# Kernel optimization log

Measured on AMD Instinct MI355X. Metric: run time of the kernel, lower is better.

Reference implementation:

```python
import jax, jax.numpy as jnp
import numpy as np

K_NN = 32          # configs['k']
LEAKY_ALPHA = 0.2  # configs['alpha']
NHEADS = 8         # all heads share gat_W0/gat_a0 in the weights dict -> tiled output
NEG_INF = -9e15    # masked-softmax fill used by dense GAT


@jax.custom_vjp
def grad_reverse(x):
    # GradientReversalLayer: identity forward, negated gradient backward
    return x

def _gr_fwd(x):
    return x, None

def _gr_bwd(res, g):
    return (-g,)

grad_reverse.defvjp(_gr_fwd, _gr_bwd)


def setup_inputs() -> dict:
    key = jax.random.key(0)
    ks = jax.random.split(key, 11)
    N, D = 6144, 512           # N = (num_domains+1)*batch_size = 4*1536
    H1, H2, G = 256, 128, 64   # hidden_layers=[256,128], gat_hidden=[64]
    C, ND = 16, 3              # num_classes, num source-domain discriminators

    def xav(k, shape):
        limit = np.float32(np.sqrt(6.0 / (shape[0] + shape[1])) * 1.414)
        return jax.random.uniform(k, shape, jnp.float32, -limit, limit)

    return {
        "x": jax.random.normal(ks[0], (N, D), jnp.float32),
        "fc_W0": xav(ks[1], (D, H1)),
        "fc_b0": jax.random.normal(ks[2], (H1,), jnp.float32) * 0.01,
        "fc_W1": xav(ks[3], (H1, H2)),
        "fc_b1": jax.random.normal(ks[4], (H2,), jnp.float32) * 0.01,
        "gat_W": xav(ks[5], (H2, G)),
        "gat_a": jax.random.normal(ks[6], (2 * G, 1), jnp.float32) * 0.1,
        "cls_W": xav(ks[7], (NHEADS * G, C)),
        "cls_b": jax.random.normal(ks[8], (C,), jnp.float32) * 0.01,
        "dsc_W": jax.random.uniform(ks[9], (ND, NHEADS * G, 2), jnp.float32),
        "dsc_b": jax.random.uniform(ks[10], (ND, 2), jnp.float32),
    }


def reference(x, fc_W0, fc_b0, fc_W1, fc_b1, gat_W, gat_a, cls_W, cls_b, dsc_W, dsc_b):
    # --- feature extractor MLP (Linear 'fc' + relu), dropout=0 / eval mode ---
    h = jax.nn.relu(x @ fc_W0 + fc_b0)
    h = jax.nn.relu(h @ fc_W1 + fc_b1)          # [N, 128]
    n = h.shape[0]

    # --- AdjacencyLayer / DistanceLayer: kNN over pairwise L2 distances ---
    sq = jnp.sum(h * h, axis=1)
    d2 = sq[:, None] + sq[None, :] - 2.0 * (h @ h.T)      # [N, N] squared dists
    d2 = d2 + jnp.eye(n, dtype=h.dtype) * 1e9             # exclude self from kNN
    _, idx = jax.lax.top_k(-jax.lax.stop_gradient(d2), K_NN)  # [N, K]
    adj = jnp.zeros((n, n), h.dtype).at[jnp.arange(n)[:, None], idx].set(1.0)
    adj = adj + jnp.eye(n, dtype=h.dtype)                 # self loops

    # --- dense GraphAttentionLayer (single shared head, tiled nheads times) ---
    Wh = h @ gat_W                                        # [N, G]
    Gd = Wh.shape[1]
    f1 = Wh @ gat_a[:Gd]                                  # [N, 1]
    f2 = Wh @ gat_a[Gd:]                                  # [N, 1]
    e = jax.nn.leaky_relu(f1 + f2.T, LEAKY_ALPHA)         # [N, N]
    att = jax.nn.softmax(jnp.where(adj > 0, e, NEG_INF), axis=1)
    hp = jax.nn.elu(att @ Wh)                             # [N, G]
    gat_out = jnp.tile(hp, (1, NHEADS))                   # concat of shared heads

    # --- class head + domain discriminators behind gradient reversal ---
    cls_logits = gat_out @ cls_W + cls_b                  # [N, C]
    rev = grad_reverse(gat_out)
    dsc_logits = jnp.einsum('nd,kdo->nko', rev, dsc_W) + dsc_b  # [N, ND, 2]
    return jnp.concatenate([cls_logits, dsc_logits.reshape(n, -1)], axis=1)
```

## Files before the change

kernel.cpp:

```cpp
#include <hip/hip_runtime.h>
#include <float.h>

#define N_PTS 6144
#define D_IN  512
#define H1_DIM 256
#define H2_DIM 128
#define G_DIM  64
#define KNN    32
#define NOUT   22

typedef short s8v __attribute__((ext_vector_type(8)));
typedef float f32x4 __attribute__((ext_vector_type(4)));
typedef unsigned u32x4 __attribute__((ext_vector_type(4)));
typedef unsigned short u16;
typedef unsigned long long u64;

__device__ __forceinline__ u16 f2bf(float f) {
  unsigned u = __float_as_uint(f);
  u += 0x7FFFu + ((u >> 16) & 1u);
  return (u16)(u >> 16);
}
__device__ __forceinline__ float bf2f(u16 s) {
  return __uint_as_float(((unsigned)s) << 16);
}
__device__ __forceinline__ void split3(float v, u16& a0, u16& a1, u16& a2) {
  a0 = f2bf(v);
  float r1 = v - bf2f(a0);
  a1 = f2bf(r1);
  a2 = f2bf(r1 - bf2f(a1));
}

template<int BM, bool AF32, bool SPLITK, bool BIAS, bool RELU, bool WF32, bool WSPLIT, bool WKEY>
__global__ __launch_bounds__(256, 4) void mfma_gemm(
    const void* __restrict__ A0any, const u16* __restrict__ A1_, const u16* __restrict__ A2_,
    const u16* __restrict__ B0_, const u16* __restrict__ B1_, const u16* __restrict__ B2_,
    const float* __restrict__ bias,
    float* __restrict__ Cf, u16* __restrict__ C0, u16* __restrict__ C1, u16* __restrict__ C2,
    int Ktot, int Ks, int ldC, size_t MN, int rowoff)
{
  const int MT = BM / 32, NT = 2;
  __shared__ u16 lds[(BM + 64) * 32 * 3];
  u16* Ap[3] = { lds, lds + BM * 32, lds + 2 * BM * 32 };
  u16* Bp[3] = { lds + 3 * BM * 32, lds + 3 * BM * 32 + 2048, lds + 3 * BM * 32 + 4096 };

  const int t = threadIdx.x;
  const int lane = t & 63, wave = t >> 6;
  const int wm = wave >> 1, wn = wave & 1;
  const int m0 = blockIdx.y * BM, n0 = blockIdx.x * 64;
  const int kz = blockIdx.z * Ks;

  f32x4 acc[MT][NT] = {};

  for (int k0 = 0; k0 < Ks; k0 += 32) {
    if (k0) __syncthreads();
    const int kb = kz + k0;
    if (AF32) {
      const float* A = (const float*)A0any;
      #pragma unroll
      for (int c0 = 0; c0 < BM * 4; c0 += 256) {
        int c = c0 + t;
        int row = c >> 2, slot = c & 3;
        const float* g = A + (size_t)(m0 + row) * Ktot + kb + slot * 8;
        f32x4 fa = *(const f32x4*)g;
        f32x4 fb = *(const f32x4*)(g + 4);
        int dst = row * 32 + ((slot ^ ((row >> 1) & 3)) << 3);
        s8v v0, v1, v2;
        #pragma unroll
        for (int e = 0; e < 4; ++e) {
          u16 a0, a1, a2; split3(fa[e], a0, a1, a2);
          v0[e] = (short)a0; v1[e] = (short)a1; v2[e] = (short)a2;
        }
        #pragma unroll
        for (int e = 0; e < 4; ++e) {
          u16 a0, a1, a2; split3(fb[e], a0, a1, a2);
          v0[4 + e] = (short)a0; v1[4 + e] = (short)a1; v2[4 + e] = (short)a2;
        }
        *(s8v*)(Ap[0] + dst) = v0;
        *(s8v*)(Ap[1] + dst) = v1;
        *(s8v*)(Ap[2] + dst) = v2;
      }
    } else {
      const u16* As[3] = { (const u16*)A0any, A1_, A2_ };
      #pragma unroll
      for (int c0 = 0; c0 < BM * 4; c0 += 256) {
        int c = c0 + t;
        int row = c >> 2, slot = c & 3;
        size_t g = (size_t)(m0 + row) * Ktot + kb + slot * 8;
        int dst = row * 32 + ((slot ^ ((row >> 1) & 3)) << 3);
        #pragma unroll
        for (int p = 0; p < 3; ++p)
          *(s8v*)(Ap[p] + dst) = *(const s8v*)(As[p] + g);
      }
    }
    {
      const u16* Bs[3] = { B0_, B1_, B2_ };
      int row = t >> 2, slot = t & 3;
      size_t g = (size_t)(n0 + row) * Ktot + kb + slot * 8;
      int dst = row * 32 + ((slot ^ ((row >> 1) & 3)) << 3);
      #pragma unroll
      for (int p = 0; p < 3; ++p)
        *(s8v*)(Bp[p] + dst) = *(const s8v*)(Bs[p] + g);
    }
    __syncthreads();

    s8v af[3][MT], bf[3][NT];
    #pragma unroll
    for (int mt = 0; mt < MT; ++mt) {
      int r = wm * (BM / 2) + mt * 16 + (lane & 15);
      int off = r * 32 + (((lane >> 4) ^ ((r >> 1) & 3)) << 3);
      #pragma unroll
      for (int p = 0; p < 3; ++p) af[p][mt] = *(const s8v*)(Ap[p] + off);
    }
    #pragma unroll
    for (int nt = 0; nt < NT; ++nt) {
      int r = wn * 32 + nt * 16 + (lane & 15);
      int off = r * 32 + (((lane >> 4) ^ ((r >> 1) & 3)) << 3);
      #pragma unroll
      for (int p = 0; p < 3; ++p) bf[p][nt] = *(const s8v*)(Bp[p] + off);
    }
    #pragma unroll
    for (int mt = 0; mt < MT; ++mt)
      #pragma unroll
      for (int nt = 0; nt < NT; ++nt) {
        f32x4 a = acc[mt][nt];
        a = __builtin_amdgcn_mfma_f32_16x16x32_bf16(af[0][mt], bf[0][nt], a, 0, 0, 0);
        a = __builtin_amdgcn_mfma_f32_16x16x32_bf16(af[0][mt], bf[1][nt], a, 0, 0, 0);
        a = __builtin_amdgcn_mfma_f32_16x16x32_bf16(af[1][mt], bf[0][nt], a, 0, 0, 0);
        a = __builtin_amdgcn_mfma_f32_16x16x32_bf16(af[1][mt], bf[1][nt], a, 0, 0, 0);
        a = __builtin_amdgcn_mfma_f32_16x16x32_bf16(af[0][mt], bf[2][nt], a, 0, 0, 0);
        a = __builtin_amdgcn_mfma_f32_16x16x32_bf16(af[2][mt], bf[0][nt], a, 0, 0, 0);
        acc[mt][nt] = a;
      }
  }

  #pragma unroll
  for (int mt = 0; mt < MT; ++mt) {
    #pragma unroll
    for (int nt = 0; nt < NT; ++nt) {
      int col = n0 + wn * 32 + nt * 16 + (lane & 15);
      float bv = (BIAS && !SPLITK) ? bias[col] : 0.f;
      float sqc = WKEY ? bias[col] : 0.f;
      #pragma unroll
      for (int v = 0; v < 4; ++v) {
        int row = m0 + wm * (BM / 2) + mt * 16 + (lane >> 4) * 4 + v;
        float val = acc[mt][nt][v] + bv;
        size_t o = (size_t)row * ldC + col;
        if (SPLITK) {
          Cf[(size_t)blockIdx.z * MN + o] = val;
        } else if (WKEY) {
          float f = fmaf(-2.f, val, sqc);
          unsigned ub = __float_as_uint(f);
          unsigned uu = (ub & 0x80000000u) ? ~ub : (ub | 0x80000000u);
          if (rowoff + row == col) uu = 0xFFFFFFFFu;
          ((unsigned*)Cf)[o] = uu;
        } else {
          if (RELU) val = fmaxf(val, 0.f);
          if (WF32) Cf[o] = val;
          if (WSPLIT) {
            u16 a0, a1, a2; split3(val, a0, a1, a2);
            C0[o] = a0; C1[o] = a1; C2[o] = a2;
          }
        }
      }
    }
  }
}

template<int S, bool BIAS, bool RELU, bool WF32, bool WSPLIT>
__global__ void combine(const float* __restrict__ P, const float* __restrict__ bias,
                        size_t MN, int Ncols,
                        float* __restrict__ Cf, u16* __restrict__ C0,
                        u16* __restrict__ C1, u16* __restrict__ C2)
{
  size_t idx = ((size_t)blockIdx.x * 256 + threadIdx.x) * 4;
  if (idx >= MN) return;
  f32x4 s = *(const f32x4*)(P + idx);
  #pragma unroll
  for (int z = 1; z < S; ++z) s += *(const f32x4*)(P + (size_t)z * MN + idx);
  int n = (int)(idx % (size_t)Ncols);
  #pragma unroll
  for (int e = 0; e < 4; ++e) {
    float v = s[e] + (BIAS ? bias[n + e] : 0.f);
    if (RELU) v = fmaxf(v, 0.f);
    if (WF32) Cf[idx + e] = v;
    if (WSPLIT) {
      u16 a0, a1, a2; split3(v, a0, a1, a2);
      C0[idx + e] = a0; C1[idx + e] = a1; C2[idx + e] = a2;
    }
  }
}

__global__ void trans_split3(const float* __restrict__ W0, u16* __restrict__ a0,
                             u16* __restrict__ a1, u16* __restrict__ a2,
                             const float* __restrict__ W1, u16* __restrict__ b0,
                             u16* __restrict__ b1, u16* __restrict__ b2,
                             const float* __restrict__ gW, u16* __restrict__ c0,
                             u16* __restrict__ c1, u16* __restrict__ c2)
{
  int id = blockIdx.x * 256 + threadIdx.x;
  const int S0 = D_IN * H1_DIM, S1 = H1_DIM * H2_DIM, S2 = H2_DIM * G_DIM;
  const float* W; u16 *p0, *p1, *p2; int K, N;
  if (id < S0)           { W = W0; p0 = a0; p1 = a1; p2 = a2; K = D_IN;   N = H1_DIM; }
  else if (id < S0 + S1) { id -= S0; W = W1; p0 = b0; p1 = b1; p2 = b2; K = H1_DIM; N = H2_DIM; }
  else if (id < S0 + S1 + S2) { id -= S0 + S1; W = gW; p0 = c0; p1 = c1; p2 = c2; K = H2_DIM; N = G_DIM; }
  else return;
  int k = id / N, n = id % N;
  u16 x0, x1, x2;
  split3(W[id], x0, x1, x2);
  size_t o = (size_t)n * K + k;
  p0[o] = x0; p1[o] = x1; p2[o] = x2;
}

__global__ void prep_head(const float* __restrict__ cW, const float* __restrict__ cb,
                          const float* __restrict__ dW, const float* __restrict__ db,
                          float* __restrict__ Wc, float* __restrict__ bc)
{
  int t = threadIdx.x;
  for (int idx = t; idx < 64 * NOUT; idx += 256) {
    int g = idx / NOUT, c = idx % NOUT;
    float s = 0.f;
    if (c < 16) {
      for (int r = 0; r < 8; ++r) s += cW[(r * 64 + g) * 16 + c];
    } else {
      int k = (c - 16) >> 1, o = (c - 16) & 1;
      for (int r = 0; r < 8; ++r) s += dW[k * 1024 + (r * 64 + g) * 2 + o];
    }
    Wc[idx] = s;
  }
  if (t < NOUT) bc[t] = (t < 16) ? cb[t] : db[t - 16];
}

__global__ void row_stats(const float* __restrict__ h, const float* __restrict__ Wh,
                          const float* __restrict__ ga, float* __restrict__ sq,
                          float* __restrict__ f1, float* __restrict__ f2)
{
  int i = blockIdx.x * 256 + threadIdx.x;
  const float* hr = h + (size_t)i * H2_DIM;
  float s = 0.f;
  for (int k = 0; k < H2_DIM; ++k) { float v = hr[k]; s = fmaf(v, v, s); }
  sq[i] = s;
  const float* wr = Wh + (size_t)i * G_DIM;
  float a = 0.f, b = 0.f;
  for (int g = 0; g < G_DIM; ++g) {
    float w = wr[g];
    a = fmaf(w, ga[g], a);
    b = fmaf(w, ga[G_DIM + g], b);
  }
  f1[i] = a; f2[i] = b;
}

__global__ __launch_bounds__(256) void topk_att(const unsigned* __restrict__ Sb,
    const float* __restrict__ f1, const float* __restrict__ f2,
    const float* __restrict__ Wh, const float* __restrict__ Wc, const float* __restrict__ bc,
    float* __restrict__ out, int m0)
{
  const int t = threadIdx.x;
  const int lane = t & 63, wv = t >> 6;
  const int row4 = blockIdx.x * 4 + wv;
  const int i = m0 + row4;
  const unsigned* Srow = Sb + (size_t)row4 * N_PTS;

  __shared__ float WcL[64 * NOUT];
  __shared__ u64 candS[4][256];
  __shared__ int neighS[4][33];
  __shared__ float attS[4][33];
  __shared__ float hpfS[4][64];

  for (int idx = t; idx < 64 * NOUT; idx += 256) WcL[idx] = Wc[idx];
  __syncthreads();

  unsigned q[24];
  #pragma unroll
  for (int c = 0; c < 24; ++c) {
    u32x4 v = *(const u32x4*)(Srow + (c << 8) + (lane << 2));
    unsigned a = v[0] < v[1] ? v[0] : v[1];
    unsigned b = v[2] < v[3] ? v[2] : v[3];
    q[c] = a < b ? a : b;
  }

  unsigned lmin = q[0];
  #pragma unroll
  for (int c = 1; c < 24; ++c) lmin = q[c] < lmin ? q[c] : lmin;

  unsigned sv = lmin;
  for (int k = 2; k <= 64; k <<= 1) {
    for (int j = k >> 1; j >= 1; j >>= 1) {
      unsigned o = __shfl_xor(sv, j);
      bool up = ((lane & k) == 0) == ((lane & j) == 0);
      sv = up ? (sv < o ? sv : o) : (sv > o ? sv : o);
    }
  }
  unsigned Q = __shfl(sv, 31);
  const unsigned s0 = __shfl(sv, 0);

  const u64 below = (lane == 0) ? 0ull : (~0ull >> (64 - lane));

  candS[wv][lane] = ~0ull;
  candS[wv][64 + lane] = ~0ull;
  candS[wv][128 + lane] = ~0ull;
  candS[wv][192 + lane] = ~0ull;
  int cnt = 0;
  #pragma unroll
  for (int c = 0; c < 24; ++c) {
    bool act = (q[c] <= Q);
    u64 mask = __ballot(act);
    if (act) {
      int pos = cnt + (int)__popcll(mask & below);
      if (pos < 64) {
        u32x4 v = *(const u32x4*)(Srow + (c << 8) + (lane << 2));
        #pragma unroll
        for (int e = 0; e < 4; ++e) {
          int j = (c << 8) + (lane << 2) + e;
          candS[wv][pos * 4 + e] = ((u64)v[e] << 13) | (unsigned)j;
        }
      }
    }
    cnt += (int)__popcll(mask);
  }

  if (cnt > 64) {
    long long lo = (long long)s0 - 1, hi = (long long)Q;
    while (hi - lo > 1) {
      long long span = hi - lo;
      unsigned m1 = (unsigned)(lo + (span >> 2));
      unsigned m2 = (unsigned)(lo + (span >> 1));
      unsigned m3 = (unsigned)(hi - (span >> 2));
      int c1 = 0, c2 = 0, c3 = 0;
      #pragma unroll
      for (int c = 0; c < 24; ++c) {
        c1 += (q[c] <= m1);
        c2 += (q[c] <= m2);
        c3 += (q[c] <= m3);
      }
      #pragma unroll
      for (int off = 32; off > 0; off >>= 1) {
        c1 += __shfl_xor(c1, off);
        c2 += __shfl_xor(c2, off);
        c3 += __shfl_xor(c3, off);
      }
      if (c1 >= KNN)       { hi = m1; }
      else if (c2 >= KNN)  { lo = m1; hi = m2; }
      else if (c3 >= KNN)  { lo = m2; hi = m3; }
      else                 { lo = m3; }
    }
    Q = (unsigned)hi;
    candS[wv][lane] = ~0ull;
    candS[wv][64 + lane] = ~0ull;
    candS[wv][128 + lane] = ~0ull;
    candS[wv][192 + lane] = ~0ull;
    cnt = 0;
    #pragma unroll
    for (int c = 0; c < 24; ++c) {
      bool act = (q[c] <= Q);
      u64 mask = __ballot(act);
      if (act) {
        int pos = cnt + (int)__popcll(mask & below);
        if (pos < 64) {
          u32x4 v = *(const u32x4*)(Srow + (c << 8) + (lane << 2));
          #pragma unroll
          for (int e = 0; e < 4; ++e) {
            int j = (c << 8) + (lane << 2) + e;
            candS[wv][pos * 4 + e] = ((u64)v[e] << 13) | (unsigned)j;
          }
        }
      }
      cnt += (int)__popcll(mask);
    }
  }

  if (cnt <= 32) {
    u64 v0 = candS[wv][2 * lane], v1 = candS[wv][2 * lane + 1];
    const int e0 = 2 * lane, e1 = e0 + 1;
    for (int k = 2; k <= 128; k <<= 1) {
      for (int j = k >> 1; j >= 2; j >>= 1) {
        int half = j >> 1;
        u64 o0 = __shfl_xor(v0, half);
        u64 o1 = __shfl_xor(v1, half);
        bool up0 = ((e0 & k) == 0) == ((e0 & j) == 0);
        bool up1 = ((e1 & k) == 0) == ((e1 & j) == 0);
        v0 = up0 ? (v0 < o0 ? v0 : o0) : (v0 > o0 ? v0 : o0);
        v1 = up1 ? (v1 < o1 ? v1 : o1) : (v1 > o1 ? v1 : o1);
      }
      bool asc = ((e0 & k) == 0);
      u64 a = v0 < v1 ? v0 : v1, b = v0 < v1 ? v1 : v0;
      v0 = asc ? a : b;
      v1 = asc ? b : a;
    }
    if (lane < 16) {
      neighS[wv][2 * lane]     = (int)(v0 & 0x1FFFu);
      neighS[wv][2 * lane + 1] = (int)(v1 & 0x1FFFu);
    }
    if (lane == 0) neighS[wv][32] = i;
  } else {
    for (int k = 2; k <= 256; k <<= 1) {
      for (int j = k >> 1; j >= 1; j >>= 1) {
        #pragma unroll
        for (int s = 0; s < 4; ++s) {
          int e = lane + s * 64;
          int p = e ^ j;
          if (p > e) {
            u64 a = candS[wv][e], b = candS[wv][p];
            bool asc = ((e & k) == 0);
            if ((a > b) == asc) { candS[wv][e] = b; candS[wv][p] = a; }
          }
        }
      }
    }
    if (lane < KNN) neighS[wv][lane] = (int)(candS[wv][lane] & 0x1FFFu);
    if (lane == 0) neighS[wv][32] = i;
  }

  {
    float e = -FLT_MAX;
    if (lane < 33) {
      float raw = f1[i] + f2[neighS[wv][lane]];
      e = raw > 0.f ? raw : 0.2f * raw;
    }
    float mx = e;
    #pragma unroll
    for (int off = 32; off > 0; off >>= 1) mx = fmaxf(mx, __shfl_xor(mx, off));
    float ex = (lane < 33) ? expf(e - mx) : 0.f;
    float sm = ex;
    #pragma unroll
    for (int off = 32; off > 0; off >>= 1) sm += __shfl_xor(sm, off);
    if (lane < 33) attS[wv][lane] = ex / sm;
  }

  {
    float s = 0.f;
    for (int m = 0; m < 33; ++m)
      s = fmaf(attS[wv][m], Wh[(size_t)neighS[wv][m] * G_DIM + lane], s);
    hpfS[wv][lane] = s > 0.f ? s : expm1f(s);
  }

  if (lane < NOUT) {
    float o = bc[lane];
    for (int g = 0; g < 64; ++g) o = fmaf(hpfS[wv][g], WcL[g * NOUT + lane], o);
    out[(size_t)i * NOUT + lane] = o;
  }
}

extern "C" void kernel_launch(void* const* d_in, const int* in_sizes, int n_in,
                              void* d_out, int out_size, void* d_ws, size_t ws_size,
                              hipStream_t stream)
{
  const float* x  = (const float*)d_in[0];
  const float* W0 = (const float*)d_in[1];
  const float* b0 = (const float*)d_in[2];
  const float* W1 = (const float*)d_in[3];
  const float* b1 = (const float*)d_in[4];
  const float* gW = (const float*)d_in[5];
  const float* ga = (const float*)d_in[6];
  const float* cW = (const float*)d_in[7];
  const float* cb = (const float*)d_in[8];
  const float* dW = (const float*)d_in[9];
  const float* db = (const float*)d_in[10];
  float* out = (float*)d_out;

  char* base = (char*)d_ws;
  char* w = base;
  auto alloc = [&](size_t bytes) { char* p = w; w += (bytes + 255) & ~(size_t)255; return p; };
  u16 *W0p[3], *W1p[3], *gWp[3], *h1p[3], *hp[3];
  for (int p = 0; p < 3; ++p) W0p[p] = (u16*)alloc((size_t)D_IN * H1_DIM * 2);
  for (int p = 0; p < 3; ++p) W1p[p] = (u16*)alloc((size_t)H1_DIM * H2_DIM * 2);
  for (int p = 0; p < 3; ++p) gWp[p] = (u16*)alloc((size_t)H2_DIM * G_DIM * 2);
  for (int p = 0; p < 3; ++p) h1p[p] = (u16*)alloc((size_t)N_PTS * H1_DIM * 2);
  for (int p = 0; p < 3; ++p) hp[p]  = (u16*)alloc((size_t)N_PTS * H2_DIM * 2);
  float* hF  = (float*)alloc((size_t)N_PTS * H2_DIM * 4);
  float* WhF = (float*)alloc((size_t)N_PTS * G_DIM * 4);
  float* sqv = (float*)alloc(N_PTS * 4);
  float* f1v = (float*)alloc(N_PTS * 4);
  float* f2v = (float*)alloc(N_PTS * 4);
  float* Wc  = (float*)alloc(64 * NOUT * 4);
  float* bc  = (float*)alloc(64 * 4);

  char* pbase = w;
  const size_t MN1 = (size_t)N_PTS * H1_DIM;
  const size_t MN2 = (size_t)N_PTS * H2_DIM;
  const size_t MN3 = (size_t)N_PTS * G_DIM;
  float* P1 = (float*)alloc(4 * MN1 * 4);
  float* P2 = (float*)alloc(4 * MN2 * 4);
  float* P3 = (float*)alloc(4 * MN3 * 4);
  float* Sb = (float*)pbase;

  size_t used_persist = (size_t)(pbase - base);
  size_t avail = (ws_size > used_persist) ? (ws_size - used_persist) / 4 : 0;
  int rowblk = 128;
  const int rcand[] = {6144, 3072, 1536, 768, 384, 256, 128};
  for (int c : rcand) { if ((size_t)c * N_PTS <= avail) { rowblk = c; break; } }

  const int TS = D_IN * H1_DIM + H1_DIM * H2_DIM + H2_DIM * G_DIM;
  trans_split3<<<(TS + 255) / 256, 256, 0, stream>>>(
      W0, W0p[0], W0p[1], W0p[2], W1, W1p[0], W1p[1], W1p[2], gW, gWp[0], gWp[1], gWp[2]);
  prep_head<<<1, 256, 0, stream>>>(cW, cb, dW, db, Wc, bc);

  mfma_gemm<64, true, true, false, false, false, false, false>
      <<<dim3(H1_DIM / 64, N_PTS / 64, 4), 256, 0, stream>>>(
      x, nullptr, nullptr, W0p[0], W0p[1], W0p[2], nullptr,
      P1, nullptr, nullptr, nullptr, D_IN, D_IN / 4, H1_DIM, MN1, 0);
  combine<4, true, true, false, true><<<(int)(MN1 / 1024), 256, 0, stream>>>(
      P1, b0, MN1, H1_DIM, nullptr, h1p[0], h1p[1], h1p[2]);

  mfma_gemm<64, false, true, false, false, false, false, false>
      <<<dim3(H2_DIM / 64, N_PTS / 64, 4), 256, 0, stream>>>(
      h1p[0], h1p[1], h1p[2], W1p[0], W1p[1], W1p[2], nullptr,
      P2, nullptr, nullptr, nullptr, H1_DIM, H1_DIM / 4, H2_DIM, MN2, 0);
  combine<4, true, true, true, true><<<(int)(MN2 / 1024), 256, 0, stream>>>(
      P2, b1, MN2, H2_DIM, hF, hp[0], hp[1], hp[2]);

  mfma_gemm<64, false, true, false, false, false, false, false>
      <<<dim3(G_DIM / 64, N_PTS / 64, 4), 256, 0, stream>>>(
      hp[0], hp[1], hp[2], gWp[0], gWp[1], gWp[2], nullptr,
      P3, nullptr, nullptr, nullptr, H2_DIM, H2_DIM / 4, G_DIM, MN3, 0);
  combine<4, false, false, true, false><<<(int)(MN3 / 1024), 256, 0, stream>>>(
      P3, nullptr, MN3, G_DIM, WhF, nullptr, nullptr, nullptr);

  row_stats<<<N_PTS / 256, 256, 0, stream>>>(hF, WhF, ga, sqv, f1v, f2v);

  for (int b = 0; b < N_PTS / rowblk; ++b) {
    mfma_gemm<128, false, false, false, false, false, false, true>
        <<<dim3(N_PTS / 64, rowblk / 128, 1), 256, 0, stream>>>(
        hp[0] + (size_t)b * rowblk * H2_DIM, hp[1] + (size_t)b * rowblk * H2_DIM,
        hp[2] + (size_t)b * rowblk * H2_DIM, hp[0], hp[1], hp[2], sqv,
        Sb, nullptr, nullptr, nullptr, H2_DIM, H2_DIM, N_PTS, 0, b * rowblk);
    topk_att<<<rowblk / 4, 256, 0, stream>>>((const unsigned*)Sb, f1v, f2v, WhF, Wc, bc, out, b * rowblk);
  }
}
```

Measured before the change: 190.0 us.

## Split each top-k row across two wavefronts and merge sorted halves

Each row's top-32 selection is now split between two wavefronts, each scanning half of the 6144 distance columns with 12 register chunks instead of 24. The two sorted 32-candidate lists go to shared memory, and a bitonic merge in the first wavefront produces the final neighbour set before attention and the output head run. This doubles the block count and halves per-wave register and scan work, aiming for more parallelism and less latency per row. In exchange it adds a block-wide barrier and a merge step, and the second wavefront sits idle during the attention phase.

```diff
diff --git a/kernel.cpp b/kernel.cpp
--- a/kernel.cpp
+++ b/kernel.cpp
@@ -256,23 +256,26 @@
 {
   const int t = threadIdx.x;
   const int lane = t & 63, wv = t >> 6;
-  const int row4 = blockIdx.x * 4 + wv;
-  const int i = m0 + row4;
-  const unsigned* Srow = Sb + (size_t)row4 * N_PTS;
+  const int rloc = wv >> 1, half = wv & 1;
+  const int row2 = blockIdx.x * 2 + rloc;
+  const int i = m0 + row2;
+  const unsigned* Srow = Sb + (size_t)row2 * N_PTS;
+  const int hbase = half * 3072;
 
   __shared__ float WcL[64 * NOUT];
   __shared__ u64 candS[4][256];
-  __shared__ int neighS[4][33];
-  __shared__ float attS[4][33];
-  __shared__ float hpfS[4][64];
+  __shared__ u64 mergeS[4][32];
+  __shared__ int neighS[2][33];
+  __shared__ float attS[2][33];
+  __shared__ float hpfS[2][64];
 
   for (int idx = t; idx < 64 * NOUT; idx += 256) WcL[idx] = Wc[idx];
   __syncthreads();
 
-  unsigned q[24];
+  unsigned q[12];
   #pragma unroll
-  for (int c = 0; c < 24; ++c) {
-    u32x4 v = *(const u32x4*)(Srow + (c << 8) + (lane << 2));
+  for (int c = 0; c < 12; ++c) {
+    u32x4 v = *(const u32x4*)(Srow + hbase + (c << 8) + (lane << 2));
     unsigned a = v[0] < v[1] ? v[0] : v[1];
     unsigned b = v[2] < v[3] ? v[2] : v[3];
     q[c] = a < b ? a : b;
@@ -280,7 +283,7 @@
 
   unsigned lmin = q[0];
   #pragma unroll
-  for (int c = 1; c < 24; ++c) lmin = q[c] < lmin ? q[c] : lmin;
+  for (int c = 1; c < 12; ++c) lmin = q[c] < lmin ? q[c] : lmin;
 
   unsigned sv = lmin;
   for (int k = 2; k <= 64; k <<= 1) {
@@ -301,16 +304,16 @@
   candS[wv][192 + lane] = ~0ull;
   int cnt = 0;
   #pragma unroll
-  for (int c = 0; c < 24; ++c) {
+  for (int c = 0; c < 12; ++c) {
     bool act = (q[c] <= Q);
     u64 mask = __ballot(act);
     if (act) {
       int pos = cnt + (int)__popcll(mask & below);
       if (pos < 64) {
-        u32x4 v = *(const u32x4*)(Srow + (c << 8) + (lane << 2));
+        u32x4 v = *(const u32x4*)(Srow + hbase + (c << 8) + (lane << 2));
         #pragma unroll
         for (int e = 0; e < 4; ++e) {
-          int j = (c << 8) + (lane << 2) + e;
+          int j = hbase + (c << 8) + (lane << 2) + e;
           candS[wv][pos * 4 + e] = ((u64)v[e] << 13) | (unsigned)j;
         }
       }
@@ -327,7 +330,7 @@
       unsigned m3 = (unsigned)(hi - (span >> 2));
       int c1 = 0, c2 = 0, c3 = 0;
       #pragma unroll
-      for (int c = 0; c < 24; ++c) {
+      for (int c = 0; c < 12; ++c) {
         c1 += (q[c] <= m1);
         c2 += (q[c] <= m2);
         c3 += (q[c] <= m3);
@@ -350,16 +353,16 @@
     candS[wv][192 + lane] = ~0ull;
     cnt = 0;
     #pragma unroll
-    for (int c = 0; c < 24; ++c) {
+    for (int c = 0; c < 12; ++c) {
       bool act = (q[c] <= Q);
       u64 mask = __ballot(act);
       if (act) {
         int pos = cnt + (int)__popcll(mask & below);
         if (pos < 64) {
-          u32x4 v = *(const u32x4*)(Srow + (c << 8) + (lane << 2));
+          u32x4 v = *(const u32x4*)(Srow + hbase + (c << 8) + (lane << 2));
           #pragma unroll
           for (int e = 0; e < 4; ++e) {
-            int j = (c << 8) + (lane << 2) + e;
+            int j = hbase + (c << 8) + (lane << 2) + e;
             candS[wv][pos * 4 + e] = ((u64)v[e] << 13) | (unsigned)j;
           }
         }
@@ -373,9 +376,9 @@
     const int e0 = 2 * lane, e1 = e0 + 1;
     for (int k = 2; k <= 128; k <<= 1) {
       for (int j = k >> 1; j >= 2; j >>= 1) {
-        int half = j >> 1;
-        u64 o0 = __shfl_xor(v0, half);
-        u64 o1 = __shfl_xor(v1, half);
+        int hf = j >> 1;
+        u64 o0 = __shfl_xor(v0, hf);
+        u64 o1 = __shfl_xor(v1, hf);
         bool up0 = ((e0 & k) == 0) == ((e0 & j) == 0);
         bool up1 = ((e1 & k) == 0) == ((e1 & j) == 0);
         v0 = up0 ? (v0 < o0 ? v0 : o0) : (v0 > o0 ? v0 : o0);
@@ -387,10 +390,9 @@
       v1 = asc ? b : a;
     }
     if (lane < 16) {
-      neighS[wv][2 * lane]     = (int)(v0 & 0x1FFFu);
-      neighS[wv][2 * lane + 1] = (int)(v1 & 0x1FFFu);
-    }
-    if (lane == 0) neighS[wv][32] = i;
+      mergeS[wv][2 * lane]     = v0;
+      mergeS[wv][2 * lane + 1] = v1;
+    }
   } else {
     for (int k = 2; k <= 256; k <<= 1) {
       for (int j = k >> 1; j >= 1; j >>= 1) {
@@ -406,37 +408,49 @@
         }
       }
     }
-    if (lane < KNN) neighS[wv][lane] = (int)(candS[wv][lane] & 0x1FFFu);
-    if (lane == 0) neighS[wv][32] = i;
-  }
-
-  {
-    float e = -FLT_MAX;
-    if (lane < 33) {
-      float raw = f1[i] + f2[neighS[wv][lane]];
-      e = raw > 0.f ? raw : 0.2f * raw;
-    }
-    float mx = e;
+    if (lane < 32) mergeS[wv][lane] = candS[wv][lane];
+  }
+  __syncthreads();
+
+  if (half == 0) {
+    u64 v = (lane < 32) ? mergeS[wv][lane] : mergeS[wv + 1][63 - lane];
     #pragma unroll
-    for (int off = 32; off > 0; off >>= 1) mx = fmaxf(mx, __shfl_xor(mx, off));
-    float ex = (lane < 33) ? expf(e - mx) : 0.f;
-    float sm = ex;
-    #pragma unroll
-    for (int off = 32; off > 0; off >>= 1) sm += __shfl_xor(sm, off);
-    if (lane < 33) attS[wv][lane] = ex / sm;
-  }
-
-  {
-    float s = 0.f;
-    for (int m = 0; m < 33; ++m)
-      s = fmaf(attS[wv][m], Wh[(size_t)neighS[wv][m] * G_DIM + lane], s);
-    hpfS[wv][lane] = s > 0.f ? s : expm1f(s);
-  }
-
-  if (lane < NOUT) {
-    float o = bc[lane];
-    for (int g = 0; g < 64; ++g) o = fmaf(hpfS[wv][g], WcL[g * NOUT + lane], o);
-    out[(size_t)i * NOUT + lane] = o;
+    for (int j = 32; j >= 1; j >>= 1) {
+      u64 o = __shfl_xor(v, j);
+      bool up = (lane & j) == 0;
+      v = up ? (v < o ? v : o) : (v > o ? v : o);
+    }
+    if (lane < KNN) neighS[rloc][lane] = (int)(v & 0x1FFFu);
+    if (lane == 0) neighS[rloc][32] = i;
+
+    {
+      float e = -FLT_MAX;
+      if (lane < 33) {
+        float raw = f1[i] + f2[neighS[rloc][lane]];
+        e = raw > 0.f ? raw : 0.2f * raw;
+      }
+      float mx = e;
+      #pragma unroll
+      for (int off = 32; off > 0; off >>= 1) mx = fmaxf(mx, __shfl_xor(mx, off));
+      float ex = (lane < 33) ? expf(e - mx) : 0.f;
+      float sm = ex;
+      #pragma unroll
+      for (int off = 32; off > 0; off >>= 1) sm += __shfl_xor(sm, off);
+      if (lane < 33) attS[rloc][lane] = ex / sm;
+    }
+
+    {
+      float s = 0.f;
+      for (int m = 0; m < 33; ++m)
+        s = fmaf(attS[rloc][m], Wh[(size_t)neighS[rloc][m] * G_DIM + lane], s);
+      hpfS[rloc][lane] = s > 0.f ? s : expm1f(s);
+    }
+
+    if (lane < NOUT) {
+      float o = bc[lane];
+      for (int g = 0; g < 64; ++g) o = fmaf(hpfS[rloc][g], WcL[g * NOUT + lane], o);
+      out[(size_t)i * NOUT + lane] = o;
+    }
   }
 }
 
@@ -523,6 +537,6 @@
         hp[0] + (size_t)b * rowblk * H2_DIM, hp[1] + (size_t)b * rowblk * H2_DIM,
         hp[2] + (size_t)b * rowblk * H2_DIM, hp[0], hp[1], hp[2], sqv,
         Sb, nullptr, nullptr, nullptr, H2_DIM, H2_DIM, N_PTS, 0, b * rowblk);
-    topk_att<<<rowblk / 4, 256, 0, stream>>>((const unsigned*)Sb, f1v, f2v, WhF, Wc, bc, out, b * rowblk);
-  }
-}
+    topk_att<<<rowblk / 2, 256, 0, stream>>>((const unsigned*)Sb, f1v, f2v, WhF, Wc, bc, out, b * rowblk);
+  }
+}
```

Result: slower. 199.9 us (+5.2%).

## Load GEMM tiles via global_load_lds and always bisect kNN threshold

Applied to the files above, without the earlier changes.

The MFMA GEMM now copies pre-split bf16 A and B tiles straight from global memory into LDS with global_load_lds. This drops the register round trip, and the XOR swizzle is applied on the source address instead. The f32-input path also uses direct-to-LDS loads for B. Separately, the kNN selection no longer uses a 64-lane bitonic sort to pick a threshold and only bisects when it overflows. It now always bisects the 32nd-smallest quantized key between the wave min and max, which removes the sort and the second candidate pass but may cost more bisection iterations.

```diff
diff --git a/kernel.cpp b/kernel.cpp
--- a/kernel.cpp
+++ b/kernel.cpp
@@ -39,9 +39,9 @@
     int Ktot, int Ks, int ldC, size_t MN, int rowoff)
 {
   const int MT = BM / 32, NT = 2;
+  const int APL = BM * 32;
+  const int BBASE = 3 * APL;
   __shared__ u16 lds[(BM + 64) * 32 * 3];
-  u16* Ap[3] = { lds, lds + BM * 32, lds + 2 * BM * 32 };
-  u16* Bp[3] = { lds + 3 * BM * 32, lds + 3 * BM * 32 + 2048, lds + 3 * BM * 32 + 4096 };
 
   const int t = threadIdx.x;
   const int lane = t & 63, wave = t >> 6;
@@ -50,6 +50,9 @@
   const int kz = blockIdx.z * Ks;
 
   f32x4 acc[MT][NT] = {};
+
+  const int pA = BM / 16;
+  const int NC = 3 * pA + 12;
 
   for (int k0 = 0; k0 < Ks; k0 += 32) {
     if (k0) __syncthreads();
@@ -75,31 +78,44 @@
           u16 a0, a1, a2; split3(fb[e], a0, a1, a2);
           v0[4 + e] = (short)a0; v1[4 + e] = (short)a1; v2[4 + e] = (short)a2;
         }
-        *(s8v*)(Ap[0] + dst) = v0;
-        *(s8v*)(Ap[1] + dst) = v1;
-        *(s8v*)(Ap[2] + dst) = v2;
+        *(s8v*)(lds + dst) = v0;
+        *(s8v*)(lds + APL + dst) = v1;
+        *(s8v*)(lds + 2 * APL + dst) = v2;
+      }
+      for (int c = wave; c < 12; c += 4) {
+        int p = c >> 2, lc = c & 3;
+        int row = lc * 16 + (lane >> 2);
+        int srcslot = (lane & 3) ^ ((row >> 1) & 3);
+        const u16* src = (p == 0) ? B0_ : (p == 1) ? B1_ : B2_;
+        const u16* g = src + (size_t)(n0 + row) * Ktot + kb + srcslot * 8;
+        __builtin_amdgcn_global_load_lds(
+            (const __attribute__((address_space(1))) unsigned*)g,
+            (__attribute__((address_space(3))) unsigned*)(lds + BBASE + p * 2048 + lc * 512),
+            16, 0, 0);
       }
     } else {
-      const u16* As[3] = { (const u16*)A0any, A1_, A2_ };
-      #pragma unroll
-      for (int c0 = 0; c0 < BM * 4; c0 += 256) {
-        int c = c0 + t;
-        int row = c >> 2, slot = c & 3;
-        size_t g = (size_t)(m0 + row) * Ktot + kb + slot * 8;
-        int dst = row * 32 + ((slot ^ ((row >> 1) & 3)) << 3);
-        #pragma unroll
-        for (int p = 0; p < 3; ++p)
-          *(s8v*)(Ap[p] + dst) = *(const s8v*)(As[p] + g);
-      }
-    }
-    {
-      const u16* Bs[3] = { B0_, B1_, B2_ };
-      int row = t >> 2, slot = t & 3;
-      size_t g = (size_t)(n0 + row) * Ktot + kb + slot * 8;
-      int dst = row * 32 + ((slot ^ ((row >> 1) & 3)) << 3);
-      #pragma unroll
-      for (int p = 0; p < 3; ++p)
-        *(s8v*)(Bp[p] + dst) = *(const s8v*)(Bs[p] + g);
+      for (int c = wave; c < NC; c += 4) {
+        const u16* src; int dstoff; int row0; int lc;
+        if (c < 3 * pA) {
+          int p = c / pA; lc = c % pA;
+          src = (p == 0) ? (const u16*)A0any : (p == 1) ? A1_ : A2_;
+          dstoff = p * APL + lc * 512;
+          row0 = m0;
+        } else {
+          int cb = c - 3 * pA;
+          int p = cb >> 2; lc = cb & 3;
+          src = (p == 0) ? B0_ : (p == 1) ? B1_ : B2_;
+          dstoff = BBASE + p * 2048 + lc * 512;
+          row0 = n0;
+        }
+        int row = lc * 16 + (lane >> 2);
+        int srcslot = (lane & 3) ^ ((row >> 1) & 3);
+        const u16* g = src + (size_t)(row0 + row) * Ktot + kb + srcslot * 8;
+        __builtin_amdgcn_global_load_lds(
+            (const __attribute__((address_space(1))) unsigned*)g,
+            (__attribute__((address_space(3))) unsigned*)(lds + dstoff),
+            16, 0, 0);
+      }
     }
     __syncthreads();
 
@@ -109,14 +125,14 @@
       int r = wm * (BM / 2) + mt * 16 + (lane & 15);
       int off = r * 32 + (((lane >> 4) ^ ((r >> 1) & 3)) << 3);
       #pragma unroll
-      for (int p = 0; p < 3; ++p) af[p][mt] = *(const s8v*)(Ap[p] + off);
+      for (int p = 0; p < 3; ++p) af[p][mt] = *(const s8v*)(lds + p * APL + off);
     }
     #pragma unroll
     for (int nt = 0; nt < NT; ++nt) {
       int r = wn * 32 + nt * 16 + (lane & 15);
       int off = r * 32 + (((lane >> 4) ^ ((r >> 1) & 3)) << 3);
       #pragma unroll
-      for (int p = 0; p < 3; ++p) bf[p][nt] = *(const s8v*)(Bp[p] + off);
+      for (int p = 0; p < 3; ++p) bf[p][nt] = *(const s8v*)(lds + BBASE + p * 2048 + off);
     }
     #pragma unroll
     for (int mt = 0; mt < MT; ++mt)
@@ -282,23 +298,44 @@
   #pragma unroll
   for (int c = 1; c < 24; ++c) lmin = q[c] < lmin ? q[c] : lmin;
 
-  unsigned sv = lmin;
-  for (int k = 2; k <= 64; k <<= 1) {
-    for (int j = k >> 1; j >= 1; j >>= 1) {
-      unsigned o = __shfl_xor(sv, j);
-      bool up = ((lane & k) == 0) == ((lane & j) == 0);
-      sv = up ? (sv < o ? sv : o) : (sv > o ? sv : o);
-    }
-  }
-  unsigned Q = __shfl(sv, 31);
-  const unsigned s0 = __shfl(sv, 0);
-
-  const u64 below = (lane == 0) ? 0ull : (~0ull >> (64 - lane));
+  unsigned mnl = lmin, mxl = lmin;
+  #pragma unroll
+  for (int off = 32; off > 0; off >>= 1) {
+    unsigned o1 = __shfl_xor(mnl, off); mnl = o1 < mnl ? o1 : mnl;
+    unsigned o2 = __shfl_xor(mxl, off); mxl = o2 > mxl ? o2 : mxl;
+  }
+
+  long long lo = (long long)mnl - 1, hi = (long long)mxl;
+  while (hi - lo > 1) {
+    long long span = hi - lo;
+    unsigned m1 = (unsigned)(lo + (span >> 2));
+    unsigned m2 = (unsigned)(lo + (span >> 1));
+    unsigned m3 = (unsigned)(hi - (span >> 2));
+    int c1 = 0, c2 = 0, c3 = 0;
+    #pragma unroll
+    for (int c = 0; c < 24; ++c) {
+      c1 += (q[c] <= m1);
+      c2 += (q[c] <= m2);
+      c3 += (q[c] <= m3);
+    }
+    #pragma unroll
+    for (int off = 32; off > 0; off >>= 1) {
+      c1 += __shfl_xor(c1, off);
+      c2 += __shfl_xor(c2, off);
+      c3 += __shfl_xor(c3, off);
+    }
+    if (c1 >= KNN)       { hi = m1; }
+    else if (c2 >= KNN)  { lo = m1; hi = m2; }
+    else if (c3 >= KNN)  { lo = m2; hi = m3; }
+    else                 { lo = m3; }
+  }
+  const unsigned Q = (unsigned)hi;
 
   candS[wv][lane] = ~0ull;
   candS[wv][64 + lane] = ~0ull;
   candS[wv][128 + lane] = ~0ull;
   candS[wv][192 + lane] = ~0ull;
+  const u64 below = (lane == 0) ? 0ull : (~0ull >> (64 - lane));
   int cnt = 0;
   #pragma unroll
   for (int c = 0; c < 24; ++c) {
@@ -316,56 +353,6 @@
       }
     }
     cnt += (int)__popcll(mask);
-  }
-
-  if (cnt > 64) {
-    long long lo = (long long)s0 - 1, hi = (long long)Q;
-    while (hi - lo > 1) {
-      long long span = hi - lo;
-      unsigned m1 = (unsigned)(lo + (span >> 2));
-      unsigned m2 = (unsigned)(lo + (span >> 1));
-      unsigned m3 = (unsigned)(hi - (span >> 2));
-      int c1 = 0, c2 = 0, c3 = 0;
-      #pragma unroll
-      for (int c = 0; c < 24; ++c) {
-        c1 += (q[c] <= m1);
-        c2 += (q[c] <= m2);
-        c3 += (q[c] <= m3);
-      }
-      #pragma unroll
-      for (int off = 32; off > 0; off >>= 1) {
-        c1 += __shfl_xor(c1, off);
-        c2 += __shfl_xor(c2, off);
-        c3 += __shfl_xor(c3, off);
-      }
-      if (c1 >= KNN)       { hi = m1; }
-      else if (c2 >= KNN)  { lo = m1; hi = m2; }
-      else if (c3 >= KNN)  { lo = m2; hi = m3; }
-      else                 { lo = m3; }
-    }
-    Q = (unsigned)hi;
-    candS[wv][lane] = ~0ull;
-    candS[wv][64 + lane] = ~0ull;
-    candS[wv][128 + lane] = ~0ull;
-    candS[wv][192 + lane] = ~0ull;
-    cnt = 0;
-    #pragma unroll
-    for (int c = 0; c < 24; ++c) {
-      bool act = (q[c] <= Q);
-      u64 mask = __ballot(act);
-      if (act) {
-        int pos = cnt + (int)__popcll(mask & below);
-        if (pos < 64) {
-          u32x4 v = *(const u32x4*)(Srow + (c << 8) + (lane << 2));
-          #pragma unroll
-          for (int e = 0; e < 4; ++e) {
-            int j = (c << 8) + (lane << 2) + e;
-            candS[wv][pos * 4 + e] = ((u64)v[e] << 13) | (unsigned)j;
-          }
-        }
-      }
-      cnt += (int)__popcll(mask);
-    }
   }
 
   if (cnt <= 32) {
```

After: 193.2 us. No clear change (+1.7%).
